# Performance work log

Hardware: AMD Instinct MI355X
Metric: run time of the kernel (lower is better)

Reference implementation:

```python
import jax, jax.numpy as jnp
import numpy as np

N = 8388608          # number of samples (2**23)
T_MAX = 100000       # number of distinct time values -> ~84 ties per time


def setup_inputs() -> dict:
    key = jax.random.key(0)
    k1, k2, k3 = jax.random.split(key, 3)
    inp = jax.random.normal(k1, (N,), dtype=jnp.float32)            # log hazards
    target = jax.random.randint(k2, (N,), 0, T_MAX, dtype=jnp.int32)  # times
    weight = jax.random.randint(k3, (N,), 0, 2, dtype=jnp.int32)      # event indicator
    return {"input": inp, "target": target, "weight": weight}


def _cox_efron_npll(log_hz, time, event):
    """Negative Cox partial log-likelihood with Efron tie correction, mean reduction.

    Faithful to torchsurv's _partial_likelihood_efron: per unique time j,
    pll_j = sum_{i in H_j} log_hz_i - sum_{l=0}^{m_j-1} log(D_j - (l/m_j)*T_j)
    where H_j = events at time j, D_j = sum of exp(log_hz) over risk set (t>=t_j),
    T_j = sum of exp(log_hz) over H_j, m_j = |H_j|; loss = -mean over j with m_j>0.
    """
    n = log_hz.shape[0]
    order = jnp.argsort(time)                       # sort by time (group-sum math is tie-order invariant)
    t = time[order]
    lh = log_hz[order]
    ev = event[order].astype(lh.dtype)

    # group id per sample: 0..(num_unique-1), padded groups beyond that are empty
    new_grp = jnp.concatenate([jnp.zeros((1,), jnp.int32), (t[1:] != t[:-1]).astype(jnp.int32)])
    seg = jnp.cumsum(new_grp)                       # [n] int32

    hz = jnp.exp(lh)
    grp_hz = jax.ops.segment_sum(hz, seg, num_segments=n)          # sum exp per time group
    denom_naive = jnp.cumsum(grp_hz[::-1])[::-1]                   # risk-set sums (suffix over groups)
    m = jax.ops.segment_sum(ev, seg, num_segments=n)               # events per group
    log_nom = jax.ops.segment_sum(lh * ev, seg, num_segments=n)    # sum of log_hz over H_j
    ties = jax.ops.segment_sum(hz * ev, seg, num_segments=n)       # sum of exp over H_j

    # rank l in [0, m_j) of each event within its group
    csum_e = jnp.cumsum(ev)
    events_before = jnp.concatenate([jnp.zeros((1,), lh.dtype), jnp.cumsum(m)[:-1]])
    rank = csum_e - 1.0 - events_before[seg]
    mg = jnp.maximum(m[seg], 1.0)
    term = jnp.where(ev > 0.0,
                     jnp.log(denom_naive[seg] - (rank / mg) * ties[seg]),
                     0.0)
    log_denom = jax.ops.segment_sum(term, seg, num_segments=n)

    include = (m > 0.0).astype(lh.dtype)
    pll = jnp.where(m > 0.0, log_nom - log_denom, 0.0)
    # reduction='mean': -pll.nanmean() over groups that contain events
    return -(jnp.sum(pll) / jnp.sum(include))


def reference(input, target, weight):
    return _cox_efron_npll(input, target, weight)
```

## Files before the change

kernel.cpp:

```cpp
#include <hip/hip_runtime.h>

#define TMAXV 100000
#define CHUNK 256
#define NCHUNK ((TMAXV + CHUNK - 1) / CHUNK)
#define WB 256
#define LOGWB 8
#define SB ((TMAXV + WB - 1) / WB)
#define TILE 4096
#define RPT 16
#define KS 8
#define CAP 4096
#define RPH (CAP / 256)

__device__ __forceinline__ float block_reduce_sum(float v, float* sdata) {
    int lane = threadIdx.x & 63;
    int wid  = threadIdx.x >> 6;
    #pragma unroll
    for (int off = 32; off > 0; off >>= 1)
        v += __shfl_down(v, off, 64);
    if (lane == 0) sdata[wid] = v;
    __syncthreads();
    if (wid == 0) {
        v = (lane < 4) ? sdata[lane] : 0.0f;
        v += __shfl_down(v, 2, 64);
        v += __shfl_down(v, 1, 64);
    }
    return v;
}


__global__ void count_kernel(const int* __restrict__ tgt,
                             int* __restrict__ blkcnt, int n, int nt) {
    __shared__ int lc[SB];
    for (int i = threadIdx.x; i < SB; i += blockDim.x) lc[i] = 0;
    __syncthreads();
    int tile = blockIdx.x;
    int lo = tile * TILE;
    int hi = min(n, lo + TILE);
    for (int i = lo + threadIdx.x; i < hi; i += blockDim.x)
        atomicAdd(&lc[tgt[i] >> LOGWB], 1);
    __syncthreads();
    for (int s = threadIdx.x; s < SB; s += blockDim.x)
        blkcnt[s * nt + tile] = lc[s];
}

__global__ void tile_scan_kernel(const int* __restrict__ blkcnt,
                                 int* __restrict__ tilebase,
                                 int* __restrict__ totals, int nt) {
    __shared__ int ls[256];
    int s   = blockIdx.x;
    int tid = threadIdx.x;
    int run = 0;
    for (int t0 = 0; t0 < nt; t0 += 256) {
        int t = t0 + tid;
        int c = (t < nt) ? blkcnt[s * nt + t] : 0;
        ls[tid] = c;
        __syncthreads();
        for (int off = 1; off < 256; off <<= 1) {
            int a = (tid >= off) ? ls[tid - off] : 0;
            __syncthreads();
            ls[tid] += a;
            __syncthreads();
        }
        int incl = ls[tid];
        int tot  = ls[255];
        if (t < nt) tilebase[s * nt + t] = run + incl - c;
        run += tot;
        __syncthreads();
    }
    if (tid == 0) totals[s] = run;
}

__global__ void bucket_base_kernel(const int* __restrict__ totals,
                                   int* __restrict__ base, int n) {
    __shared__ int ls[512];
    int tid = threadIdx.x;
    int c = (tid < SB) ? totals[tid] : 0;
    ls[tid] = c;
    __syncthreads();
    for (int off = 1; off < 512; off <<= 1) {
        int a = (tid >= off) ? ls[tid - off] : 0;
        __syncthreads();
        ls[tid] += a;
        __syncthreads();
    }
    if (tid < SB) base[tid] = ls[tid] - c;
    if (tid == 0) base[SB] = n;
}

__global__ void scatter_kernel(const float* __restrict__ lh,
                               const int*   __restrict__ tgt,
                               const int*   __restrict__ ev,
                               const int*   __restrict__ tilebase,
                               const int*   __restrict__ base,
                               float* __restrict__ val,
                               unsigned char* __restrict__ slotArr,
                               double* __restrict__ acc, int n, int nt) {
    __shared__ float fv[TILE];
    __shared__ unsigned char fs[TILE];
    __shared__ int lcnt[SB];
    __shared__ int pfx[SB];
    __shared__ int lrank[SB];
    __shared__ int tb[SB];
    __shared__ int ls[512];
    __shared__ float sdata[4];
    int tid  = threadIdx.x;
    int tile = blockIdx.x;
    int lo   = tile * TILE;
    int cnt_here = min(TILE, n - lo);

    for (int s = tid; s < SB; s += 256) {
        lcnt[s]  = 0;
        lrank[s] = 0;
        tb[s]    = base[s] + tilebase[s * nt + tile];
    }
    __syncthreads();

    float    rv[RPT];
    unsigned rt[RPT];
    float xl = 0.f;
    #pragma unroll
    for (int k = 0; k < RPT; ++k) {
        int i = lo + k * 256 + tid;
        if (i < n) {
            int t = tgt[i];
            int e = ev[i] & 1;
            float x = lh[i];
            float h = __expf(x);
            rv[k] = e ? -h : h;
            rt[k] = (unsigned)t;
            if (e) xl += x;
            atomicAdd(&lcnt[t >> LOGWB], 1);
        } else {
            rt[k] = 0xFFFFFFFFu;
        }
    }
    __syncthreads();

    int c0   = (tid < SB) ? lcnt[tid] : 0;
    int idx1 = tid + 256;
    int c1   = (idx1 < SB) ? lcnt[idx1] : 0;
    ls[tid]  = c0;
    ls[idx1] = c1;
    __syncthreads();
    for (int off = 1; off < 512; off <<= 1) {
        int a0 = (tid  >= off) ? ls[tid  - off] : 0;
        int a1 = (idx1 >= off) ? ls[idx1 - off] : 0;
        __syncthreads();
        ls[tid]  += a0;
        ls[idx1] += a1;
        __syncthreads();
    }
    if (tid  < SB) pfx[tid]  = ls[tid]  - c0;
    if (idx1 < SB) pfx[idx1] = ls[idx1] - c1;
    __syncthreads();

    #pragma unroll
    for (int k = 0; k < RPT; ++k) {
        if (rt[k] != 0xFFFFFFFFu) {
            int b = (int)(rt[k] >> LOGWB);
            int r = atomicAdd(&lrank[b], 1);
            int pos = pfx[b] + r;
            fv[pos] = rv[k];
            fs[pos] = (unsigned char)(rt[k] & (WB - 1));
        }
    }
    __syncthreads();

    for (int p = tid; p < cnt_here; p += 256) {
        int loB = 0, hiB = SB;
        #pragma unroll
        for (int it = 0; it < 9; ++it) {
            int mid = (loB + hiB) >> 1;
            if (pfx[mid] <= p) loB = mid; else hiB = mid;
        }
        int dst = tb[loB] + (p - pfx[loB]);
        val[dst]     = fv[p];
        slotArr[dst] = fs[p];
    }

    float rl = block_reduce_sum(xl, sdata);
    if (tid == 0) atomicAdd(&acc[2], (double)rl);
}

__global__ void bucket_hist_kernel(const float* __restrict__ val,
                                   const unsigned char* __restrict__ slotArr,
                                   const int* __restrict__ base,
                                   float* __restrict__ partials) {
    __shared__ float fv[CAP];
    __shared__ unsigned cnt[WB];
    __shared__ unsigned rankc[WB];
    __shared__ unsigned pfx[WB];
    __shared__ unsigned ls[WB];
    int tid = threadIdx.x;
    int b   = blockIdx.x >> 3;
    int k   = blockIdx.x & (KS - 1);
    int lo0 = base[b], len = base[b + 1] - lo0;
    int lo  = lo0 + (int)(((long long)len * k) / KS);
    int hi  = lo0 + (int)(((long long)len * (k + 1)) / KS);

    float sh = 0.f, cm = 0.f, th = 0.f;

    for (int c0 = lo; c0 < hi; c0 += CAP) {
        int c1 = min(hi, c0 + CAP);
        cnt[tid] = 0; rankc[tid] = 0;
        __syncthreads();

        float rv[RPH];
        int   rs[RPH];
        #pragma unroll
        for (int u = 0; u < RPH; ++u) {
            int i = c0 + u * 256 + tid;
            if (i < c1) {
                rv[u] = val[i];
                rs[u] = (int)slotArr[i];
                atomicAdd(&cnt[rs[u]], 1u);
            } else {
                rs[u] = -1;
            }
        }
        __syncthreads();

        unsigned c = cnt[tid];
        ls[tid] = c;
        __syncthreads();
        for (int off = 1; off < 256; off <<= 1) {
            unsigned a = (tid >= off) ? ls[tid - off] : 0u;
            __syncthreads();
            ls[tid] += a;
            __syncthreads();
        }
        pfx[tid] = ls[tid] - c;
        __syncthreads();

        #pragma unroll
        for (int u = 0; u < RPH; ++u) {
            if (rs[u] >= 0) {
                unsigned r = atomicAdd(&rankc[rs[u]], 1u);
                fv[pfx[rs[u]] + r] = rv[u];
            }
        }
        __syncthreads();

        int s0 = (int)pfx[tid], e0 = s0 + (int)cnt[tid];
        for (int p = s0; p < e0; ++p) {
            float v = fv[p];
            float h = fabsf(v);
            sh += h;
            if (__float_as_uint(v) >> 31) { cm += 1.0f; th += h; }
        }
        __syncthreads();
    }

    float* pbase = partials + (size_t)blockIdx.x * 3 * WB;
    pbase[0 * WB + tid] = sh;
    pbase[1 * WB + tid] = cm;
    pbase[2 * WB + tid] = th;
}

__global__ void merge_kernel(const float* __restrict__ partials,
                             float* __restrict__ sum_hz,
                             float* __restrict__ mcnt,
                             float* __restrict__ ties,
                             float* __restrict__ chunk_sum) {
    __shared__ float sdata[4];
    int tid = threadIdx.x;
    int b   = blockIdx.x;
    float sh = 0.f, cm = 0.f, th = 0.f;
    #pragma unroll
    for (int k = 0; k < KS; ++k) {
        const float* pbase = partials + (size_t)(b * KS + k) * 3 * WB;
        sh += pbase[0 * WB + tid];
        cm += pbase[1 * WB + tid];
        th += pbase[2 * WB + tid];
    }
    int t = (b << LOGWB) + tid;
    float shv = (t < TMAXV) ? sh : 0.f;
    if (t < TMAXV) {
        sum_hz[t] = sh;
        mcnt[t]   = cm;
        ties[t]   = th;
    }
    float cs = block_reduce_sum(shv, sdata);
    if (tid == 0) chunk_sum[b] = cs;
}

__global__ void chunk_scan_kernel(const float* __restrict__ chunk_sum,
                                  double* __restrict__ chunk_off) {
    __shared__ double ds[512];
    int tid = threadIdx.x;
    double own = (tid < NCHUNK) ? (double)chunk_sum[tid] : 0.0;
    ds[tid] = own;
    __syncthreads();
    for (int off = 1; off < 512; off <<= 1) {
        double add = (tid + off < 512) ? ds[tid + off] : 0.0;
        __syncthreads();
        ds[tid] += add;
        __syncthreads();
    }
    if (tid < NCHUNK) chunk_off[tid] = ds[tid] - own;
}

__global__ void pll_suffix_kernel(const float* __restrict__ sum_hz,
                                  const float* __restrict__ mcnt,
                                  const float* __restrict__ ties,
                                  const double* __restrict__ chunk_off,
                                  double* __restrict__ acc) {
    __shared__ float sf[CHUNK];
    __shared__ float sdata[4];
    __shared__ float sdata2[4];
    int tid = threadIdx.x;
    int t   = blockIdx.x * CHUNK + tid;
    float v = (t < TMAXV) ? sum_hz[t] : 0.0f;
    sf[tid] = v;
    __syncthreads();
    for (int off = 1; off < CHUNK; off <<= 1) {
        float add = (tid + off < CHUNK) ? sf[tid + off] : 0.0f;
        __syncthreads();
        sf[tid] += add;
        __syncthreads();
    }
    float pll = 0.0f, inc = 0.0f;
    if (t < TMAXV) {
        float mv = mcnt[t];
        if (mv > 0.5f) {
            float D    = (float)(chunk_off[blockIdx.x] + (double)sf[tid]);
            float T    = ties[t];
            int   mi   = (int)(mv + 0.5f);
            float step = T / mv;
            float s = 0.0f;
            for (int l = 0; l < mi; ++l)
                s += __logf(D - (float)l * step);
            pll = -s;
            inc = 1.0f;
        }
    }
    float rp = block_reduce_sum(pll, sdata);
    __syncthreads();
    float ri = block_reduce_sum(inc, sdata2);
    if (threadIdx.x == 0) {
        atomicAdd(&acc[0], (double)rp);
        atomicAdd(&acc[1], (double)ri);
    }
}

__global__ void finalize_kernel(const double* __restrict__ acc,
                                float* __restrict__ out) {
    double cnt = acc[1];
    out[0] = (cnt > 0.0) ? (float)(-(acc[0] + acc[2]) / cnt) : 0.0f;
}

__global__ void hist_kernel(const float* __restrict__ lh,
                            const int*   __restrict__ tgt,
                            const int*   __restrict__ ev,
                            float* __restrict__ sum_hz,
                            float* __restrict__ mcnt,
                            float* __restrict__ log_nom,
                            float* __restrict__ ties,
                            int n) {
    int i = blockIdx.x * blockDim.x + threadIdx.x;
    if (i >= n) return;
    float x = lh[i];
    int   t = tgt[i];
    int   e = ev[i];
    float h = __expf(x);
    unsafeAtomicAdd(&sum_hz[t], h);
    if (e) {
        unsafeAtomicAdd(&mcnt[t], 1.0f);
        unsafeAtomicAdd(&log_nom[t], x);
        unsafeAtomicAdd(&ties[t], h);
    }
}

__global__ void chunk_sum_kernel(const float* __restrict__ sum_hz,
                                 float* __restrict__ chunk_sum) {
    __shared__ float sdata[4];
    int i = blockIdx.x * CHUNK + threadIdx.x;
    float v = (i < TMAXV) ? sum_hz[i] : 0.0f;
    v = block_reduce_sum(v, sdata);
    if (threadIdx.x == 0) chunk_sum[blockIdx.x] = v;
}

__global__ void pll_kernel(const float* __restrict__ mcnt,
                           const float* __restrict__ log_nom,
                           const float* __restrict__ ties,
                           const float* __restrict__ sum_hz,
                           const double* __restrict__ chunk_off,
                           double* __restrict__ acc) {
    __shared__ float sf[CHUNK];
    __shared__ float sdata[4];
    __shared__ float sdata2[4];
    int tid = threadIdx.x;
    int t   = blockIdx.x * CHUNK + tid;
    float v = (t < TMAXV) ? sum_hz[t] : 0.0f;
    sf[tid] = v;
    __syncthreads();
    for (int off = 1; off < CHUNK; off <<= 1) {
        float add = (tid + off < CHUNK) ? sf[tid + off] : 0.0f;
        __syncthreads();
        sf[tid] += add;
        __syncthreads();
    }
    float pll = 0.0f, inc = 0.0f;
    if (t < TMAXV) {
        float mv = mcnt[t];
        if (mv > 0.5f) {
            float D    = (float)(chunk_off[blockIdx.x] + (double)sf[tid]);
            float T    = ties[t];
            int   mi   = (int)(mv + 0.5f);
            float step = T / mv;
            float s = 0.0f;
            for (int l = 0; l < mi; ++l)
                s += __logf(D - (float)l * step);
            pll = log_nom[t] - s;
            inc = 1.0f;
        }
    }
    float rp = block_reduce_sum(pll, sdata);
    __syncthreads();
    float ri = block_reduce_sum(inc, sdata2);
    if (threadIdx.x == 0) {
        atomicAdd(&acc[0], (double)rp);
        atomicAdd(&acc[1], (double)ri);
    }
}

extern "C" void kernel_launch(void* const* d_in, const int* in_sizes, int n_in,
                              void* d_out, int out_size, void* d_ws, size_t ws_size,
                              hipStream_t stream) {
    const float* lh  = (const float*)d_in[0];
    const int*   tgt = (const int*)d_in[1];
    const int*   ev  = (const int*)d_in[2];
    float*       out = (float*)d_out;
    int n  = in_sizes[0];
    int nt = (n + TILE - 1) / TILE;

    char* ws = (char*)d_ws;
    size_t off = 0;
    auto take = [&](size_t bytes, size_t align) {
        off = (off + align - 1) & ~(align - 1);
        size_t r = off; off += bytes; return r;
    };
    size_t o_acc    = take(32, 16);
    size_t o_sum    = take((size_t)TMAXV * 4, 16);
    size_t o_m      = take((size_t)TMAXV * 4, 16);
    size_t o_ties   = take((size_t)TMAXV * 4, 16);
    size_t o_base   = take((size_t)(SB + 1) * 4, 4);
    size_t o_totals = take((size_t)SB * 4, 4);
    size_t o_csum   = take((size_t)NCHUNK * 4, 16);
    size_t o_coff   = take((size_t)NCHUNK * 8, 8);
    size_t o_blkcnt = take((size_t)nt * SB * 4, 16);
    size_t o_tbase  = take((size_t)nt * SB * 4, 16);
    size_t o_val    = take((size_t)n * 4, 16);
    size_t o_slot   = take((size_t)n, 16);
    size_t o_part   = take((size_t)SB * KS * 3 * WB * 4, 16);
    size_t need     = off;

    if (ws_size >= need) {
        double* acc      = (double*)(ws + o_acc);
        float*  sum_hz   = (float*)(ws + o_sum);
        float*  mcnt     = (float*)(ws + o_m);
        float*  ties     = (float*)(ws + o_ties);
        int*    base     = (int*)(ws + o_base);
        int*    totals   = (int*)(ws + o_totals);
        float*  chunk_sum= (float*)(ws + o_csum);
        double* chunk_off= (double*)(ws + o_coff);
        int*    blkcnt   = (int*)(ws + o_blkcnt);
        int*    tilebase = (int*)(ws + o_tbase);
        float*  val      = (float*)(ws + o_val);
        unsigned char* slotArr = (unsigned char*)(ws + o_slot);
        float*  partials = (float*)(ws + o_part);

        hipMemsetAsync(d_ws, 0, 32, stream);

        count_kernel<<<nt, 256, 0, stream>>>(tgt, blkcnt, n, nt);
        tile_scan_kernel<<<SB, 256, 0, stream>>>(blkcnt, tilebase, totals, nt);
        bucket_base_kernel<<<1, 512, 0, stream>>>(totals, base, n);
        scatter_kernel<<<nt, 256, 0, stream>>>(lh, tgt, ev, tilebase, base, val, slotArr, acc, n, nt);
        bucket_hist_kernel<<<SB * KS, 256, 0, stream>>>(val, slotArr, base, partials);
        merge_kernel<<<SB, 256, 0, stream>>>(partials, sum_hz, mcnt, ties, chunk_sum);
        chunk_scan_kernel<<<1, 512, 0, stream>>>(chunk_sum, chunk_off);
        pll_suffix_kernel<<<NCHUNK, 256, 0, stream>>>(sum_hz, mcnt, ties, chunk_off, acc);
        finalize_kernel<<<1, 1, 0, stream>>>(acc, out);
    } else {
        size_t f = 0;
        auto ftake = [&](size_t bytes, size_t align) {
            f = (f + align - 1) & ~(align - 1);
            size_t r = f; f += bytes; return r;
        };
        size_t f_acc  = ftake(32, 16);
        size_t f_sum  = ftake((size_t)TMAXV * 4, 16);
        size_t f_m    = ftake((size_t)TMAXV * 4, 16);
        size_t f_ln   = ftake((size_t)TMAXV * 4, 16);
        size_t f_ties = ftake((size_t)TMAXV * 4, 16);
        size_t zb     = f;
        size_t f_csum = ftake((size_t)NCHUNK * 4, 16);
        size_t f_coff = ftake((size_t)NCHUNK * 8, 8);

        double* acc     = (double*)(ws + f_acc);
        float*  sum_hz  = (float*)(ws + f_sum);
        float*  mcnt    = (float*)(ws + f_m);
        float*  log_nom = (float*)(ws + f_ln);
        float*  ties    = (float*)(ws + f_ties);
        float*  chunk_sum = (float*)(ws + f_csum);
        double* chunk_off = (double*)(ws + f_coff);

        hipMemsetAsync(d_ws, 0, zb, stream);

        hist_kernel<<<(n + 255) / 256, 256, 0, stream>>>(lh, tgt, ev, sum_hz, mcnt, log_nom, ties, n);
        chunk_sum_kernel<<<NCHUNK, 256, 0, stream>>>(sum_hz, chunk_sum);
        chunk_scan_kernel<<<1, 512, 0, stream>>>(chunk_sum, chunk_off);
        pll_kernel<<<NCHUNK, 256, 0, stream>>>(mcnt, log_nom, ties, sum_hz, chunk_off, acc);
        finalize_kernel<<<1, 1, 0, stream>>>(acc, out);
    }
}
```

Baseline: 246.0 us.

## Pack slot and event into hazard float bits; reuse per-tile counts in scatter

```diff
diff --git a/kernel.cpp b/kernel.cpp
--- a/kernel.cpp
+++ b/kernel.cpp
@@ -12,6 +12,7 @@
 #define CAP 4096
 #define RPH (CAP / 256)
 
+
 __device__ __forceinline__ float block_reduce_sum(float v, float* sdata) {
     int lane = threadIdx.x & 63;
     int wid  = threadIdx.x >> 6;
@@ -91,14 +92,12 @@
 __global__ void scatter_kernel(const float* __restrict__ lh,
                                const int*   __restrict__ tgt,
                                const int*   __restrict__ ev,
+                               const int*   __restrict__ blkcnt,
                                const int*   __restrict__ tilebase,
                                const int*   __restrict__ base,
-                               float* __restrict__ val,
-                               unsigned char* __restrict__ slotArr,
+                               unsigned* __restrict__ val,
                                double* __restrict__ acc, int n, int nt) {
-    __shared__ float fv[TILE];
-    __shared__ unsigned char fs[TILE];
-    __shared__ int lcnt[SB];
+    __shared__ unsigned fu[TILE];
     __shared__ int pfx[SB];
     __shared__ int lrank[SB];
     __shared__ int tb[SB];
@@ -109,15 +108,29 @@
     int lo   = tile * TILE;
     int cnt_here = min(TILE, n - lo);
 
+    int c0   = (tid < SB)  ? blkcnt[tid  * nt + tile] : 0;
+    int idx1 = tid + 256;
+    int c1   = (idx1 < SB) ? blkcnt[idx1 * nt + tile] : 0;
     for (int s = tid; s < SB; s += 256) {
-        lcnt[s]  = 0;
         lrank[s] = 0;
         tb[s]    = base[s] + tilebase[s * nt + tile];
     }
-    __syncthreads();
-
-    float    rv[RPT];
-    unsigned rt[RPT];
+    ls[tid]  = c0;
+    ls[idx1] = c1;
+    __syncthreads();
+    for (int off = 1; off < 512; off <<= 1) {
+        int a0 = (tid  >= off) ? ls[tid  - off] : 0;
+        int a1 = (idx1 >= off) ? ls[idx1 - off] : 0;
+        __syncthreads();
+        ls[tid]  += a0;
+        ls[idx1] += a1;
+        __syncthreads();
+    }
+    if (tid  < SB) pfx[tid]  = ls[tid]  - c0;
+    if (idx1 < SB) pfx[idx1] = ls[idx1] - c1;
+
+    unsigned rb[RPT];
+    int      rk[RPT];
     float xl = 0.f;
     #pragma unroll
     for (int k = 0; k < RPT; ++k) {
@@ -127,42 +140,23 @@
             int e = ev[i] & 1;
             float x = lh[i];
             float h = __expf(x);
-            rv[k] = e ? -h : h;
-            rt[k] = (unsigned)t;
+            unsigned bits = (__float_as_uint(h) & 0x7FFFFF00u)
+                          | (unsigned)(t & (WB - 1))
+                          | ((unsigned)e << 31);
+            rb[k] = bits;
+            rk[k] = t >> LOGWB;
             if (e) xl += x;
-            atomicAdd(&lcnt[t >> LOGWB], 1);
         } else {
-            rt[k] = 0xFFFFFFFFu;
-        }
-    }
-    __syncthreads();
-
-    int c0   = (tid < SB) ? lcnt[tid] : 0;
-    int idx1 = tid + 256;
-    int c1   = (idx1 < SB) ? lcnt[idx1] : 0;
-    ls[tid]  = c0;
-    ls[idx1] = c1;
-    __syncthreads();
-    for (int off = 1; off < 512; off <<= 1) {
-        int a0 = (tid  >= off) ? ls[tid  - off] : 0;
-        int a1 = (idx1 >= off) ? ls[idx1 - off] : 0;
-        __syncthreads();
-        ls[tid]  += a0;
-        ls[idx1] += a1;
-        __syncthreads();
-    }
-    if (tid  < SB) pfx[tid]  = ls[tid]  - c0;
-    if (idx1 < SB) pfx[idx1] = ls[idx1] - c1;
+            rk[k] = -1;
+        }
+    }
     __syncthreads();
 
     #pragma unroll
     for (int k = 0; k < RPT; ++k) {
-        if (rt[k] != 0xFFFFFFFFu) {
-            int b = (int)(rt[k] >> LOGWB);
-            int r = atomicAdd(&lrank[b], 1);
-            int pos = pfx[b] + r;
-            fv[pos] = rv[k];
-            fs[pos] = (unsigned char)(rt[k] & (WB - 1));
+        if (rk[k] >= 0) {
+            int r = atomicAdd(&lrank[rk[k]], 1);
+            fu[pfx[rk[k]] + r] = rb[k];
         }
     }
     __syncthreads();
@@ -174,20 +168,17 @@
             int mid = (loB + hiB) >> 1;
             if (pfx[mid] <= p) loB = mid; else hiB = mid;
         }
-        int dst = tb[loB] + (p - pfx[loB]);
-        val[dst]     = fv[p];
-        slotArr[dst] = fs[p];
+        val[tb[loB] + (p - pfx[loB])] = fu[p];
     }
 
     float rl = block_reduce_sum(xl, sdata);
     if (tid == 0) atomicAdd(&acc[2], (double)rl);
 }
 
-__global__ void bucket_hist_kernel(const float* __restrict__ val,
-                                   const unsigned char* __restrict__ slotArr,
+__global__ void bucket_hist_kernel(const unsigned* __restrict__ val,
                                    const int* __restrict__ base,
                                    float* __restrict__ partials) {
-    __shared__ float fv[CAP];
+    __shared__ unsigned fv[CAP];
     __shared__ unsigned cnt[WB];
     __shared__ unsigned rankc[WB];
     __shared__ unsigned pfx[WB];
@@ -206,14 +197,14 @@
         cnt[tid] = 0; rankc[tid] = 0;
         __syncthreads();
 
-        float rv[RPH];
-        int   rs[RPH];
+        unsigned rv[RPH];
+        int      rs[RPH];
         #pragma unroll
         for (int u = 0; u < RPH; ++u) {
             int i = c0 + u * 256 + tid;
             if (i < c1) {
                 rv[u] = val[i];
-                rs[u] = (int)slotArr[i];
+                rs[u] = (int)(rv[u] & (WB - 1));
                 atomicAdd(&cnt[rs[u]], 1u);
             } else {
                 rs[u] = -1;
@@ -244,10 +235,10 @@
 
         int s0 = (int)pfx[tid], e0 = s0 + (int)cnt[tid];
         for (int p = s0; p < e0; ++p) {
-            float v = fv[p];
-            float h = fabsf(v);
+            unsigned bits = fv[p];
+            float h = fabsf(__uint_as_float(bits));
             sh += h;
-            if (__float_as_uint(v) >> 31) { cm += 1.0f; th += h; }
+            if (bits >> 31) { cm += 1.0f; th += h; }
         }
         __syncthreads();
     }
@@ -452,32 +443,30 @@
     size_t o_blkcnt = take((size_t)nt * SB * 4, 16);
     size_t o_tbase  = take((size_t)nt * SB * 4, 16);
     size_t o_val    = take((size_t)n * 4, 16);
-    size_t o_slot   = take((size_t)n, 16);
     size_t o_part   = take((size_t)SB * KS * 3 * WB * 4, 16);
     size_t need     = off;
 
     if (ws_size >= need) {
-        double* acc      = (double*)(ws + o_acc);
-        float*  sum_hz   = (float*)(ws + o_sum);
-        float*  mcnt     = (float*)(ws + o_m);
-        float*  ties     = (float*)(ws + o_ties);
-        int*    base     = (int*)(ws + o_base);
-        int*    totals   = (int*)(ws + o_totals);
-        float*  chunk_sum= (float*)(ws + o_csum);
-        double* chunk_off= (double*)(ws + o_coff);
-        int*    blkcnt   = (int*)(ws + o_blkcnt);
-        int*    tilebase = (int*)(ws + o_tbase);
-        float*  val      = (float*)(ws + o_val);
-        unsigned char* slotArr = (unsigned char*)(ws + o_slot);
-        float*  partials = (float*)(ws + o_part);
+        double*   acc      = (double*)(ws + o_acc);
+        float*    sum_hz   = (float*)(ws + o_sum);
+        float*    mcnt     = (float*)(ws + o_m);
+        float*    ties     = (float*)(ws + o_ties);
+        int*      base     = (int*)(ws + o_base);
+        int*      totals   = (int*)(ws + o_totals);
+        float*    chunk_sum= (float*)(ws + o_csum);
+        double*   chunk_off= (double*)(ws + o_coff);
+        int*      blkcnt   = (int*)(ws + o_blkcnt);
+        int*      tilebase = (int*)(ws + o_tbase);
+        unsigned* val      = (unsigned*)(ws + o_val);
+        float*    partials = (float*)(ws + o_part);
 
         hipMemsetAsync(d_ws, 0, 32, stream);
 
         count_kernel<<<nt, 256, 0, stream>>>(tgt, blkcnt, n, nt);
         tile_scan_kernel<<<SB, 256, 0, stream>>>(blkcnt, tilebase, totals, nt);
         bucket_base_kernel<<<1, 512, 0, stream>>>(totals, base, n);
-        scatter_kernel<<<nt, 256, 0, stream>>>(lh, tgt, ev, tilebase, base, val, slotArr, acc, n, nt);
-        bucket_hist_kernel<<<SB * KS, 256, 0, stream>>>(val, slotArr, base, partials);
+        scatter_kernel<<<nt, 256, 0, stream>>>(lh, tgt, ev, blkcnt, tilebase, base, val, acc, n, nt);
+        bucket_hist_kernel<<<SB * KS, 256, 0, stream>>>(val, base, partials);
         merge_kernel<<<SB, 256, 0, stream>>>(partials, sum_hz, mcnt, ties, chunk_sum);
         chunk_scan_kernel<<<1, 512, 0, stream>>>(chunk_sum, chunk_off);
         pll_suffix_kernel<<<NCHUNK, 256, 0, stream>>>(sum_hz, mcnt, ties, chunk_off, acc);
```

New measurement: 242.9 us. About the same (-1.3%).
